# Optimization experiments

Measured on AMD Instinct MI355X. Metric: run time of the kernel, lower is better.

Reference implementation:

```python
import jax, jax.numpy as jnp
import numpy as np

H = 8       # n_heads
E = 128     # embedding_size (= per-head dim)
NEG = -1000000000.0


def setup_inputs() -> dict:
    key = jax.random.key(0)
    ks = jax.random.split(key, 12)
    b, n = 8, 1024
    x = jax.random.normal(ks[0], (b, n, E), dtype=jnp.float32)
    dist = jax.random.normal(ks[1], (b, n, n), dtype=jnp.float32)
    mask = jax.random.randint(ks[2], (b, n), 0, 2).astype(jnp.float32)
    s = 1.0 / np.sqrt(E)
    Wq = jax.random.normal(ks[3], (E, H * E), dtype=jnp.float32) * s
    Wk = jax.random.normal(ks[4], (E, H * E), dtype=jnp.float32) * s
    Wv = jax.random.normal(ks[5], (E, H * E), dtype=jnp.float32) * s
    bq = jnp.zeros((H * E,), jnp.float32)
    bk = jnp.zeros((H * E,), jnp.float32)
    bv = jnp.zeros((H * E,), jnp.float32)
    Wo = jax.random.normal(ks[6], (H * E, E), dtype=jnp.float32) * (1.0 / np.sqrt(H * E))
    bo = jnp.zeros((E,), jnp.float32)
    return {"x": x, "dist": dist, "mask": mask, "Wq": Wq, "bq": bq,
            "Wk": Wk, "bk": bk, "Wv": Wv, "bv": bv, "Wo": Wo, "bo": bo}


def reference(x, dist, mask, Wq, bq, Wk, bk, Wv, bv, Wo, bo):
    b, n, e = x.shape
    scale = e ** (-0.5)
    # project and split heads: [b, n, H*E] -> [b, H, n, E]
    def heads(W, bias):
        return (x @ W + bias).reshape(b, n, H, e).transpose(0, 2, 1, 3)
    q = heads(Wq, bq) * mask[:, None, :, None]
    k = heads(Wk, bk) * mask[:, None, :, None]
    v = heads(Wv, bv) * mask[:, None, :, None]
    # scores with additive distance bias broadcast over heads
    a = jnp.einsum('bhqe,bhke->bhqk', q * scale, k) + dist[:, None, :, :]
    am = jnp.einsum('bq,bk->bqk', mask, mask)[:, None, :, :]  # [b,1,n,n]
    a = jnp.where(am == 0, NEG, a)
    a = jax.nn.softmax(a, axis=-1)
    a = jnp.where(am == 0, 0.0, a)
    y = jnp.einsum('bhqk,bhke->bhqe', a, v)
    y = y.transpose(0, 2, 1, 3).reshape(b, n, H * e)
    y = y @ Wo + bo
    return y * mask[:, :, None]
```

## Files before the change

### kernel.cpp

```cpp
#include <hip/hip_runtime.h>
#include <hip/hip_bf16.h>

#define NH 8
#define ED 128
#define NB 8
#define NN 1024

typedef __attribute__((ext_vector_type(8))) short s16x8;
typedef __attribute__((ext_vector_type(8))) __bf16 bf16x8_t;
typedef __attribute__((ext_vector_type(4))) float f32x4;

static __device__ __forceinline__ unsigned short f2bf(float f) {
    union { float f; unsigned u; } v; v.f = f;
    unsigned r = v.u + 0x7fffu + ((v.u >> 16) & 1u);
    return (unsigned short)(r >> 16);
}

static __device__ __forceinline__ f32x4 mfma16(s16x8 a, s16x8 b, f32x4 c) {
    return __builtin_amdgcn_mfma_f32_16x16x32_bf16(
        __builtin_bit_cast(bf16x8_t, a), __builtin_bit_cast(bf16x8_t, b), c, 0, 0, 0);
}

__global__ __launch_bounds__(256) void prep_kernel(
    const float* __restrict__ x,
    const float* __restrict__ Wq, const float* __restrict__ Wk,
    const float* __restrict__ Wv, const float* __restrict__ Wo,
    unsigned short* __restrict__ xb,
    unsigned short* __restrict__ wqt, unsigned short* __restrict__ wkt,
    unsigned short* __restrict__ wvt, unsigned short* __restrict__ wot) {
    int bid = blockIdx.x, tid = threadIdx.x;
    if (bid < 1024) {
        int i = bid * 256 + tid;
        float4 v = ((const float4*)x)[i];
        unsigned long long pk = (unsigned long long)f2bf(v.x)
                              | ((unsigned long long)f2bf(v.y) << 16)
                              | ((unsigned long long)f2bf(v.z) << 32)
                              | ((unsigned long long)f2bf(v.w) << 48);
        ((unsigned long long*)xb)[i] = pk;
        return;
    }
    const float* in; unsigned short* outp; int rows_in, cols_in, i;
    if (bid < 1536)      { in = Wq; outp = wqt; rows_in = 128;  cols_in = 1024; i = (bid - 1024) * 256 + tid; }
    else if (bid < 2048) { in = Wk; outp = wkt; rows_in = 128;  cols_in = 1024; i = (bid - 1536) * 256 + tid; }
    else if (bid < 2560) { in = Wv; outp = wvt; rows_in = 128;  cols_in = 1024; i = (bid - 2048) * 256 + tid; }
    else                 { in = Wo; outp = wot; rows_in = 1024; cols_in = 128;  i = (bid - 2560) * 256 + tid; }
    int c = i / rows_in;
    int r = i - c * rows_in;
    outp[i] = f2bf(in[(size_t)r * cols_in + c]);
}

__global__ __launch_bounds__(256) void qkv_kernel(
    const unsigned short* __restrict__ xb,
    const unsigned short* __restrict__ wqt,
    const unsigned short* __restrict__ wkt,
    const unsigned short* __restrict__ wvt,
    const float* __restrict__ bq, const float* __restrict__ bk, const float* __restrict__ bv,
    unsigned short* __restrict__ q_ws,
    unsigned short* __restrict__ k_ws,
    unsigned short* __restrict__ v_ws) {
    int bid = blockIdx.x;
    int mt = bid / 24, c = bid % 24;
    int which = c >> 3;
    int c0 = (c & 7) * 128;
    int m0 = mt * 128;
    int tid = threadIdx.x;
    int w = tid >> 6, lane = tid & 63, g = lane >> 4, r15 = lane & 15;
    int wr = (w >> 1) * 64, wc = (w & 1) * 64;

    const unsigned short* wt = (which == 0) ? wqt : (which == 1) ? wkt : wvt;
    const float* bias = (which == 0) ? bq : (which == 1) ? bk : bv;

    const f32x4 fzero = {0.f, 0.f, 0.f, 0.f};
    f32x4 acc[4][4];
#pragma unroll
    for (int i = 0; i < 4; i++)
#pragma unroll
        for (int j = 0; j < 4; j++) acc[i][j] = fzero;

#pragma unroll
    for (int kf = 0; kf < 4; kf++) {
        s16x8 af[4], bfr[4];
#pragma unroll
        for (int mf = 0; mf < 4; mf++)
            af[mf] = *(const s16x8*)(xb + (size_t)(m0 + wr + mf * 16 + r15) * ED + kf * 32 + g * 8);
#pragma unroll
        for (int nf = 0; nf < 4; nf++)
            bfr[nf] = *(const s16x8*)(wt + (size_t)(c0 + wc + nf * 16 + r15) * ED + kf * 32 + g * 8);
#pragma unroll
        for (int mf = 0; mf < 4; mf++)
#pragma unroll
            for (int nf = 0; nf < 4; nf++)
                acc[mf][nf] = mfma16(af[mf], bfr[nf], acc[mf][nf]);
    }

    float scale = (which == 0) ? 0.08838834764831845f : 1.0f;

#pragma unroll
    for (int nf = 0; nf < 4; nf++) {
        int col = c0 + wc + nf * 16 + r15;
        float bv_ = bias[col];
        int hh = col >> 7, e = col & 127;
#pragma unroll
        for (int mf = 0; mf < 4; mf++) {
#pragma unroll
            for (int rr = 0; rr < 4; rr++) {
                int row = m0 + wr + mf * 16 + g * 4 + rr;
                int bb = row >> 10, n = row & 1023;
                float val = (acc[mf][nf][rr] + bv_) * scale;
                if (which == 2)
                    v_ws[((size_t)(bb * NH + hh) * ED + e) * NN + n] = f2bf(val);
                else if (which == 0)
                    q_ws[((size_t)(bb * NH + hh) * NN + n) * ED + e] = f2bf(val);
                else
                    k_ws[((size_t)(bb * NH + hh) * NN + n) * ED + e] = f2bf(val);
            }
        }
    }
}

__global__ __launch_bounds__(512) void attn_kernel(
    const unsigned short* __restrict__ q_ws,
    const unsigned short* __restrict__ k_ws,
    const unsigned short* __restrict__ v_ws,
    const float* __restrict__ dist,
    const float* __restrict__ mask,
    unsigned short* __restrict__ y_ws) {
    int p = blockIdx.x;
    int xcd = p & 7, j = p >> 3;
    int bh = xcd * 8 + (j >> 3);
    int qt = j & 7;
    int b = bh >> 3;
    int q0 = qt * 128;

    int tid = threadIdx.x;
    int w = tid >> 6, lane = tid & 63, g = lane >> 4, r15 = lane & 15;

    __shared__ __align__(16) unsigned short Kl[64 * 128];
    __shared__ __align__(16) unsigned short Vt[128 * 64];
    __shared__ __align__(16) unsigned short Pl[8][16 * 64];
    __shared__ float mk_s[NN];

    const unsigned short* kbase = k_ws + (size_t)bh * NN * ED;
    const unsigned short* vbase = v_ws + (size_t)bh * ED * NN;
    const float* mbase = mask + b * NN;
    const float* drow = dist + (size_t)b * NN * NN + (size_t)(q0 + w * 16 + g * 4) * NN + r15;

    int krow0 = tid >> 4, kseg = tid & 15;
    int vrow0 = tid >> 3, vseg = tid & 7;

    mk_s[tid] = mbase[tid];
    mk_s[tid + 512] = mbase[tid + 512];

    s16x8 qf[4];
    const unsigned short* qb = q_ws + ((size_t)bh * NN + q0 + w * 16 + r15) * ED;
#pragma unroll
    for (int kf = 0; kf < 4; kf++) qf[kf] = *(const s16x8*)(qb + kf * 32 + g * 8);

    const f32x4 fzero = {0.f, 0.f, 0.f, 0.f};
    f32x4 o[8];
#pragma unroll
    for (int i = 0; i < 8; i++) o[i] = fzero;
    float l_r[4] = {0.f, 0.f, 0.f, 0.f};

    s16x8 kreg[2], vreg[2];
#pragma unroll
    for (int it = 0; it < 2; ++it) {
        kreg[it] = *(const s16x8*)(kbase + (size_t)(krow0 + it * 32) * ED + kseg * 8);
        vreg[it] = *(const s16x8*)(vbase + (size_t)(vrow0 + it * 64) * NN + vseg * 8);
    }

    for (int kt = 0; kt < 16; ++kt) {
        int k0 = kt * 64;
#pragma unroll
        for (int it = 0; it < 2; ++it) {
            int row = krow0 + it * 32;
            int byt = row * 256 + kseg * 16; byt ^= (row & 7) << 4;
            *(s16x8*)((char*)Kl + byt) = kreg[it];
            int e = vrow0 + it * 64;
            int vbyt = e * 128 + vseg * 16; vbyt ^= (e & 7) << 4;
            *(s16x8*)((char*)Vt + vbyt) = vreg[it];
        }
        __syncthreads();

        if (kt < 15) {
            int k0n = k0 + 64;
#pragma unroll
            for (int it = 0; it < 2; ++it) {
                kreg[it] = *(const s16x8*)(kbase + (size_t)(k0n + krow0 + it * 32) * ED + kseg * 8);
                vreg[it] = *(const s16x8*)(vbase + (size_t)(vrow0 + it * 64) * NN + k0n + vseg * 8);
            }
        }

        float dvv[4][4];
#pragma unroll
        for (int nf = 0; nf < 4; nf++)
#pragma unroll
            for (int rr = 0; rr < 4; rr++)
                dvv[nf][rr] = drow[(size_t)rr * NN + k0 + nf * 16];
        float mkf[4];
#pragma unroll
        for (int nf = 0; nf < 4; nf++) mkf[nf] = mk_s[k0 + nf * 16 + r15];

        f32x4 s[4];
#pragma unroll
        for (int nf = 0; nf < 4; nf++) s[nf] = fzero;
#pragma unroll
        for (int kf = 0; kf < 4; kf++) {
#pragma unroll
            for (int nf = 0; nf < 4; nf++) {
                int key = nf * 16 + r15;
                int byt = (key * 256 + kf * 64 + g * 16) ^ ((key & 7) << 4);
                s16x8 kb = *(const s16x8*)((const char*)Kl + byt);
                s[nf] = mfma16(qf[kf], kb, s[nf]);
            }
        }

#pragma unroll
        for (int nf = 0; nf < 4; nf++) {
#pragma unroll
            for (int rr = 0; rr < 4; rr++) {
                float pv = __expf(s[nf][rr] + dvv[nf][rr] - 16.0f) * mkf[nf];
                s[nf][rr] = pv;
                l_r[rr] += pv;
            }
        }

        unsigned short* pw = &Pl[w][0];
#pragma unroll
        for (int nf = 0; nf < 4; nf++) {
#pragma unroll
            for (int rr = 0; rr < 4; rr++) {
                int row = g * 4 + rr;
                int key = nf * 16 + r15;
                int byt = (row * 128 + key * 2) ^ ((row & 7) << 4);
                *(unsigned short*)((char*)pw + byt) = f2bf(s[nf][rr]);
            }
        }

#pragma unroll
        for (int kf2 = 0; kf2 < 2; kf2++) {
            int ba = (r15 * 128 + (kf2 * 32 + g * 8) * 2) ^ ((r15 & 7) << 4);
            s16x8 pa = *(const s16x8*)((const char*)pw + ba);
#pragma unroll
            for (int nf = 0; nf < 8; nf++) {
                int e = nf * 16 + r15;
                int bb2 = (e * 128 + (kf2 * 32 + g * 8) * 2) ^ ((e & 7) << 4);
                s16x8 vb = *(const s16x8*)((const char*)Vt + bb2);
                o[nf] = mfma16(pa, vb, o[nf]);
            }
        }
        __syncthreads();
    }

#pragma unroll
    for (int rr = 0; rr < 4; rr++) {
        float ps = l_r[rr];
        ps += __shfl_xor(ps, 1, 64);
        ps += __shfl_xor(ps, 2, 64);
        ps += __shfl_xor(ps, 4, 64);
        ps += __shfl_xor(ps, 8, 64);
        float inv = (ps > 0.f) ? 1.0f / ps : 0.f;
        int row_g = q0 + w * 16 + g * 4 + rr;
        size_t base = ((size_t)b * NN + row_g) * (NH * ED) + (bh & 7) * ED;
#pragma unroll
        for (int nf = 0; nf < 8; nf++)
            y_ws[base + nf * 16 + r15] = f2bf(o[nf][rr] * inv);
    }
}

__global__ __launch_bounds__(256) void oproj_kernel(
    const unsigned short* __restrict__ y_ws,
    const unsigned short* __restrict__ wot,
    const float* __restrict__ bo,
    const float* __restrict__ mask,
    float* __restrict__ outp) {
    int bid = blockIdx.x;
    int mt = bid >> 1, nt = bid & 1;
    int m0 = mt * 64, c0 = nt * 64;
    int tid = threadIdx.x;
    int w = tid >> 6, lane = tid & 63, g = lane >> 4, r15 = lane & 15;

    const f32x4 fzero = {0.f, 0.f, 0.f, 0.f};
    f32x4 acc[4];
#pragma unroll
    for (int i = 0; i < 4; i++) acc[i] = fzero;

    const unsigned short* arow = y_ws + (size_t)(m0 + w * 16 + r15) * (NH * ED);
    for (int kt = 0; kt < 32; ++kt) {
        s16x8 af = *(const s16x8*)(arow + kt * 32 + g * 8);
#pragma unroll
        for (int nf = 0; nf < 4; nf++) {
            s16x8 bfr = *(const s16x8*)(wot + (size_t)(c0 + nf * 16 + r15) * (NH * ED) + kt * 32 + g * 8);
            acc[nf] = mfma16(af, bfr, acc[nf]);
        }
    }
#pragma unroll
    for (int nf = 0; nf < 4; nf++) {
        int col = c0 + nf * 16 + r15;
        float bias = bo[col];
#pragma unroll
        for (int rr = 0; rr < 4; rr++) {
            int token = m0 + w * 16 + g * 4 + rr;
            outp[(size_t)token * ED + col] = (acc[nf][rr] + bias) * mask[token];
        }
    }
}

extern "C" void kernel_launch(void* const* d_in, const int* in_sizes, int n_in,
                              void* d_out, int out_size, void* d_ws, size_t ws_size,
                              hipStream_t stream) {
    const float* x    = (const float*)d_in[0];
    const float* dist = (const float*)d_in[1];
    const float* mask = (const float*)d_in[2];
    const float* Wq   = (const float*)d_in[3];
    const float* bq   = (const float*)d_in[4];
    const float* Wk   = (const float*)d_in[5];
    const float* bk   = (const float*)d_in[6];
    const float* Wv   = (const float*)d_in[7];
    const float* bv   = (const float*)d_in[8];
    const float* Wo   = (const float*)d_in[9];
    const float* bo   = (const float*)d_in[10];
    float* outp = (float*)d_out;

    char* ws = (char*)d_ws;
    unsigned short* xb   = (unsigned short*)(ws);
    unsigned short* wqt  = (unsigned short*)(ws + (2u << 20));
    unsigned short* wkt  = (unsigned short*)(ws + (2u << 20) + (256u << 10));
    unsigned short* wvt  = (unsigned short*)(ws + (2u << 20) + (512u << 10));
    unsigned short* wot  = (unsigned short*)(ws + (2u << 20) + (768u << 10));
    unsigned short* q_ws = (unsigned short*)(ws + (3u << 20));
    unsigned short* k_ws = (unsigned short*)(ws + (19u << 20));
    unsigned short* v_ws = (unsigned short*)(ws + (35u << 20));
    unsigned short* y_ws = (unsigned short*)(ws + (51u << 20));

    prep_kernel<<<3072, 256, 0, stream>>>(x, Wq, Wk, Wv, Wo, xb, wqt, wkt, wvt, wot);
    qkv_kernel<<<1536, 256, 0, stream>>>(xb, wqt, wkt, wvt, bq, bk, bv, q_ws, k_ws, v_ws);
    attn_kernel<<<512, 512, 0, stream>>>(q_ws, k_ws, v_ws, dist, mask, y_ws);
    oproj_kernel<<<256, 256, 0, stream>>>(y_ws, wot, bo, mask, outp);
}
```

Measured before the change: 154.7 us.

## Rework attention kernel to 32x32 MFMA with register-resident P and 256-row tiles

Rewrites the attention kernel to use 32x32x16 bf16 MFMA, computing S transposed (K as A operand) so the probabilities stay in registers and are repacked with cvt_pk and cross-half shuffles instead of going through a shared-memory P buffer. Each block now handles 256 query rows, halving the grid to 256 blocks so each K/V tile load is reused by more queries, and dist is read with vectorized float4 loads. Block-to-(batch,head) mapping changes to interleave batches across XCDs. The trade-off is fewer blocks than CUs (256 on a part with more compute units) and higher register pressure.

```diff
diff --git a/kernel.cpp b/kernel.cpp
--- a/kernel.cpp
+++ b/kernel.cpp
@@ -9,6 +9,8 @@
 typedef __attribute__((ext_vector_type(8))) short s16x8;
 typedef __attribute__((ext_vector_type(8))) __bf16 bf16x8_t;
 typedef __attribute__((ext_vector_type(4))) float f32x4;
+typedef __attribute__((ext_vector_type(16))) float f32x16;
+typedef __attribute__((ext_vector_type(4))) unsigned int u32x4;
 
 static __device__ __forceinline__ unsigned short f2bf(float f) {
     union { float f; unsigned u; } v; v.f = f;
@@ -19,6 +21,17 @@
 static __device__ __forceinline__ f32x4 mfma16(s16x8 a, s16x8 b, f32x4 c) {
     return __builtin_amdgcn_mfma_f32_16x16x32_bf16(
         __builtin_bit_cast(bf16x8_t, a), __builtin_bit_cast(bf16x8_t, b), c, 0, 0, 0);
+}
+
+static __device__ __forceinline__ f32x16 mfma32(s16x8 a, s16x8 b, f32x16 c) {
+    return __builtin_amdgcn_mfma_f32_32x32x16_bf16(
+        __builtin_bit_cast(bf16x8_t, a), __builtin_bit_cast(bf16x8_t, b), c, 0, 0, 0);
+}
+
+static __device__ __forceinline__ unsigned cvtpk(float lo, float hi) {
+    unsigned r;
+    asm("v_cvt_pk_bf16_f32 %0, %1, %2" : "=v"(r) : "v"(lo), "v"(hi));
+    return r;
 }
 
 __global__ __launch_bounds__(256) void prep_kernel(
@@ -126,145 +139,144 @@
     const float* __restrict__ mask,
     unsigned short* __restrict__ y_ws) {
     int p = blockIdx.x;
-    int xcd = p & 7, j = p >> 3;
-    int bh = xcd * 8 + (j >> 3);
-    int qt = j & 7;
-    int b = bh >> 3;
-    int q0 = qt * 128;
+    int b = p & 7, j = p >> 3;
+    int head = j >> 2, qt = j & 3;
+    int bh = b * NH + head;
+    int q0 = qt * 256;
 
     int tid = threadIdx.x;
-    int w = tid >> 6, lane = tid & 63, g = lane >> 4, r15 = lane & 15;
-
-    __shared__ __align__(16) unsigned short Kl[64 * 128];
-    __shared__ __align__(16) unsigned short Vt[128 * 64];
-    __shared__ __align__(16) unsigned short Pl[8][16 * 64];
-    __shared__ float mk_s[NN];
+    int w = tid >> 6, lane = tid & 63;
+    int e31 = lane & 31, h = lane >> 5;
+    bool h0 = (h == 0);
+
+    __shared__ __align__(16) unsigned short Kl[8192];
+    __shared__ __align__(16) unsigned short Vl[8192];
+    __shared__ __align__(16) float mk_s[NN];
 
     const unsigned short* kbase = k_ws + (size_t)bh * NN * ED;
     const unsigned short* vbase = v_ws + (size_t)bh * ED * NN;
-    const float* mbase = mask + b * NN;
-    const float* drow = dist + (size_t)b * NN * NN + (size_t)(q0 + w * 16 + g * 4) * NN + r15;
-
-    int krow0 = tid >> 4, kseg = tid & 15;
-    int vrow0 = tid >> 3, vseg = tid & 7;
-
-    mk_s[tid] = mbase[tid];
-    mk_s[tid + 512] = mbase[tid + 512];
-
-    s16x8 qf[4];
-    const unsigned short* qb = q_ws + ((size_t)bh * NN + q0 + w * 16 + r15) * ED;
-#pragma unroll
-    for (int kf = 0; kf < 4; kf++) qf[kf] = *(const s16x8*)(qb + kf * 32 + g * 8);
-
-    const f32x4 fzero = {0.f, 0.f, 0.f, 0.f};
-    f32x4 o[8];
-#pragma unroll
-    for (int i = 0; i < 8; i++) o[i] = fzero;
-    float l_r[4] = {0.f, 0.f, 0.f, 0.f};
-
-    s16x8 kreg[2], vreg[2];
-#pragma unroll
-    for (int it = 0; it < 2; ++it) {
-        kreg[it] = *(const s16x8*)(kbase + (size_t)(krow0 + it * 32) * ED + kseg * 8);
-        vreg[it] = *(const s16x8*)(vbase + (size_t)(vrow0 + it * 64) * NN + vseg * 8);
-    }
+
+    mk_s[tid] = mask[b * NN + tid];
+    mk_s[tid + 512] = mask[b * NN + tid + 512];
+
+    int qrow = q0 + w * 32 + e31;
+    const float* drow = dist + ((size_t)b * NN + qrow) * NN;
+
+    s16x8 qf[8];
+    const unsigned short* qb = q_ws + ((size_t)bh * NN + qrow) * ED + h * 8;
+#pragma unroll
+    for (int es = 0; es < 8; ++es) qf[es] = *(const s16x8*)(qb + es * 16);
+
+    const f32x16 fz16 = {0.f,0.f,0.f,0.f,0.f,0.f,0.f,0.f,0.f,0.f,0.f,0.f,0.f,0.f,0.f,0.f};
+    f32x16 o0 = fz16, o1 = fz16, o2 = fz16, o3 = fz16;
+    float l_r = 0.f;
+
+    int k_key = tid >> 3, k_e8 = tid & 7;
+    const unsigned short* kgsrc = kbase + k_key * ED + k_e8 * 8;
+    int k_wb0 = ((k_e8 * 2 + (k_key >> 5)) * 32 + (k_key & 31)) * 16;
+    int k_wb1 = (((k_e8 + 8) * 2 + (k_key >> 5)) * 32 + (k_key & 31)) * 16;
+    int v_e = tid >> 2, v_k8 = tid & 3;
+    const unsigned short* vgsrc = vbase + (size_t)v_e * NN + v_k8 * 8;
+    int v_wb0 = (v_k8 * 128 + v_e) * 16;
+    int v_wb1 = ((v_k8 + 4) * 128 + v_e) * 16;
+
+    const char* Kp = (const char*)Kl + h * 1024 + e31 * 16;
+    const char* Vp = (const char*)Vl + h * 2048 + e31 * 16;
+
+    s16x8 kreg0 = *(const s16x8*)(kgsrc);
+    s16x8 kreg1 = *(const s16x8*)(kgsrc + 64);
+    s16x8 vreg0 = *(const s16x8*)(vgsrc);
+    s16x8 vreg1 = *(const s16x8*)(vgsrc + 32);
 
     for (int kt = 0; kt < 16; ++kt) {
         int k0 = kt * 64;
-#pragma unroll
-        for (int it = 0; it < 2; ++it) {
-            int row = krow0 + it * 32;
-            int byt = row * 256 + kseg * 16; byt ^= (row & 7) << 4;
-            *(s16x8*)((char*)Kl + byt) = kreg[it];
-            int e = vrow0 + it * 64;
-            int vbyt = e * 128 + vseg * 16; vbyt ^= (e & 7) << 4;
-            *(s16x8*)((char*)Vt + vbyt) = vreg[it];
-        }
+        *(s16x8*)((char*)Kl + k_wb0) = kreg0;
+        *(s16x8*)((char*)Kl + k_wb1) = kreg1;
+        *(s16x8*)((char*)Vl + v_wb0) = vreg0;
+        *(s16x8*)((char*)Vl + v_wb1) = vreg1;
         __syncthreads();
 
         if (kt < 15) {
-            int k0n = k0 + 64;
-#pragma unroll
-            for (int it = 0; it < 2; ++it) {
-                kreg[it] = *(const s16x8*)(kbase + (size_t)(k0n + krow0 + it * 32) * ED + kseg * 8);
-                vreg[it] = *(const s16x8*)(vbase + (size_t)(vrow0 + it * 64) * NN + k0n + vseg * 8);
+            const unsigned short* kn = kgsrc + (size_t)(kt + 1) * 64 * ED;
+            kreg0 = *(const s16x8*)(kn);
+            kreg1 = *(const s16x8*)(kn + 64);
+            const unsigned short* vn = vgsrc + k0 + 64;
+            vreg0 = *(const s16x8*)(vn);
+            vreg1 = *(const s16x8*)(vn + 32);
+        }
+
+        f32x16 sA0 = fz16, sA1 = fz16;
+#pragma unroll
+        for (int es = 0; es < 8; ++es) {
+            s16x8 kb0 = *(const s16x8*)(Kp + es * 2048);
+            s16x8 kb1 = *(const s16x8*)(Kp + es * 2048 + 512);
+            sA0 = mfma32(kb0, qf[es], sA0);
+            sA1 = mfma32(kb1, qf[es], sA1);
+        }
+
+        float pp[32];
+#pragma unroll
+        for (int kf = 0; kf < 2; ++kf) {
+#pragma unroll
+            for (int rc = 0; rc < 4; ++rc) {
+                int cb = k0 + kf * 32 + rc * 8 + 4 * h;
+                f32x4 d4 = *(const f32x4*)(drow + cb);
+                f32x4 m4 = *(const f32x4*)(&mk_s[cb]);
+#pragma unroll
+                for (int jj = 0; jj < 4; ++jj) {
+                    float sv = kf ? sA1[rc * 4 + jj] : sA0[rc * 4 + jj];
+                    float pv = __expf(sv + d4[jj] - 16.0f) * m4[jj];
+                    pp[kf * 16 + rc * 4 + jj] = pv;
+                    l_r += pv;
+                }
             }
         }
 
-        float dvv[4][4];
-#pragma unroll
-        for (int nf = 0; nf < 4; nf++)
-#pragma unroll
-            for (int rr = 0; rr < 4; rr++)
-                dvv[nf][rr] = drow[(size_t)rr * NN + k0 + nf * 16];
-        float mkf[4];
-#pragma unroll
-        for (int nf = 0; nf < 4; nf++) mkf[nf] = mk_s[k0 + nf * 16 + r15];
-
-        f32x4 s[4];
-#pragma unroll
-        for (int nf = 0; nf < 4; nf++) s[nf] = fzero;
-#pragma unroll
-        for (int kf = 0; kf < 4; kf++) {
-#pragma unroll
-            for (int nf = 0; nf < 4; nf++) {
-                int key = nf * 16 + r15;
-                int byt = (key * 256 + kf * 64 + g * 16) ^ ((key & 7) << 4);
-                s16x8 kb = *(const s16x8*)((const char*)Kl + byt);
-                s[nf] = mfma16(qf[kf], kb, s[nf]);
+#pragma unroll
+        for (int kf = 0; kf < 2; ++kf) {
+#pragma unroll
+            for (int ks2 = 0; ks2 < 2; ++ks2) {
+                const float* pb = &pp[kf * 16 + ks2 * 8];
+                unsigned X0 = cvtpk(pb[0], pb[1]);
+                unsigned X1 = cvtpk(pb[2], pb[3]);
+                unsigned Y0 = cvtpk(pb[4], pb[5]);
+                unsigned Y1 = cvtpk(pb[6], pb[7]);
+                unsigned sx0 = (unsigned)__shfl_xor((int)X0, 32, 64);
+                unsigned sx1 = (unsigned)__shfl_xor((int)X1, 32, 64);
+                unsigned sy0 = (unsigned)__shfl_xor((int)Y0, 32, 64);
+                unsigned sy1 = (unsigned)__shfl_xor((int)Y1, 32, 64);
+                u32x4 pw;
+                pw[0] = h0 ? X0 : sy0;
+                pw[1] = h0 ? X1 : sy1;
+                pw[2] = h0 ? sx0 : Y0;
+                pw[3] = h0 ? sx1 : Y1;
+                s16x8 pa = __builtin_bit_cast(s16x8, pw);
+                int kstep = kf * 2 + ks2;
+                const char* vp = Vp + kstep * 4096;
+                o0 = mfma32(pa, *(const s16x8*)(vp), o0);
+                o1 = mfma32(pa, *(const s16x8*)(vp + 512), o1);
+                o2 = mfma32(pa, *(const s16x8*)(vp + 1024), o2);
+                o3 = mfma32(pa, *(const s16x8*)(vp + 1536), o3);
             }
         }
-
-#pragma unroll
-        for (int nf = 0; nf < 4; nf++) {
-#pragma unroll
-            for (int rr = 0; rr < 4; rr++) {
-                float pv = __expf(s[nf][rr] + dvv[nf][rr] - 16.0f) * mkf[nf];
-                s[nf][rr] = pv;
-                l_r[rr] += pv;
-            }
-        }
-
-        unsigned short* pw = &Pl[w][0];
-#pragma unroll
-        for (int nf = 0; nf < 4; nf++) {
-#pragma unroll
-            for (int rr = 0; rr < 4; rr++) {
-                int row = g * 4 + rr;
-                int key = nf * 16 + r15;
-                int byt = (row * 128 + key * 2) ^ ((row & 7) << 4);
-                *(unsigned short*)((char*)pw + byt) = f2bf(s[nf][rr]);
-            }
-        }
-
-#pragma unroll
-        for (int kf2 = 0; kf2 < 2; kf2++) {
-            int ba = (r15 * 128 + (kf2 * 32 + g * 8) * 2) ^ ((r15 & 7) << 4);
-            s16x8 pa = *(const s16x8*)((const char*)pw + ba);
-#pragma unroll
-            for (int nf = 0; nf < 8; nf++) {
-                int e = nf * 16 + r15;
-                int bb2 = (e * 128 + (kf2 * 32 + g * 8) * 2) ^ ((e & 7) << 4);
-                s16x8 vb = *(const s16x8*)((const char*)Vt + bb2);
-                o[nf] = mfma16(pa, vb, o[nf]);
-            }
-        }
         __syncthreads();
     }
 
-#pragma unroll
-    for (int rr = 0; rr < 4; rr++) {
-        float ps = l_r[rr];
-        ps += __shfl_xor(ps, 1, 64);
-        ps += __shfl_xor(ps, 2, 64);
-        ps += __shfl_xor(ps, 4, 64);
-        ps += __shfl_xor(ps, 8, 64);
-        float inv = (ps > 0.f) ? 1.0f / ps : 0.f;
-        int row_g = q0 + w * 16 + g * 4 + rr;
-        size_t base = ((size_t)b * NN + row_g) * (NH * ED) + (bh & 7) * ED;
-#pragma unroll
-        for (int nf = 0; nf < 8; nf++)
-            y_ws[base + nf * 16 + r15] = f2bf(o[nf][rr] * inv);
+    float lt = l_r + __shfl_xor(l_r, 32, 64);
+    float inv = (lt > 0.f) ? 1.0f / lt : 0.f;
+#pragma unroll
+    for (int rc = 0; rc < 4; ++rc) {
+#pragma unroll
+        for (int jj = 0; jj < 4; ++jj) {
+            int qq = jj + 8 * rc + 4 * h;
+            float iq = __shfl(inv, qq, 64);
+            int row = q0 + w * 32 + qq;
+            size_t base = ((size_t)b * NN + row) * (NH * ED) + head * ED + e31;
+            y_ws[base]      = f2bf(o0[rc * 4 + jj] * iq);
+            y_ws[base + 32] = f2bf(o1[rc * 4 + jj] * iq);
+            y_ws[base + 64] = f2bf(o2[rc * 4 + jj] * iq);
+            y_ws[base + 96] = f2bf(o3[rc * 4 + jj] * iq);
+        }
     }
 }
 
@@ -335,6 +347,6 @@
 
     prep_kernel<<<3072, 256, 0, stream>>>(x, Wq, Wk, Wv, Wo, xb, wqt, wkt, wvt, wot);
     qkv_kernel<<<1536, 256, 0, stream>>>(xb, wqt, wkt, wvt, bq, bk, bv, q_ws, k_ws, v_ws);
-    attn_kernel<<<512, 512, 0, stream>>>(q_ws, k_ws, v_ws, dist, mask, y_ws);
+    attn_kernel<<<256, 512, 0, stream>>>(q_ws, k_ws, v_ws, dist, mask, y_ws);
     oproj_kernel<<<256, 256, 0, stream>>>(y_ws, wot, bo, mask, outp);
 }
```

Measured after the change: 153.6 us. No clear change (-0.8%).
